# Kernel optimization log

Hardware: AMD Instinct MI355X
Metric: run time of the kernel (lower is better)

Reference implementation:

```python
import jax, jax.numpy as jnp
import numpy as np

NUM_CODEBOOK = 2048
EMBED_DIM = 64
BETA = 0.25


def _l2norm(x, eps=1e-12):
    # F.normalize(x, dim=1): x / max(||x||, eps)
    n = jnp.sqrt(jnp.sum(x * x, axis=1, keepdims=True))
    return x / jnp.maximum(n, eps)


def setup_inputs() -> dict:
    key = jax.random.key(0)
    k1, k2 = jax.random.split(key)
    z = jax.random.normal(k1, (16, EMBED_DIM, 64, 64), dtype=jnp.float32)
    # xavier_normal_ init for (K, d) embedding weight
    std = float(np.sqrt(2.0 / (NUM_CODEBOOK + EMBED_DIM)))
    codebook = jax.random.normal(k2, (NUM_CODEBOOK, EMBED_DIM), dtype=jnp.float32) * std
    return {"z": z, "codebook": codebook}


def reference(z, codebook):
    b, d, h, w = z.shape
    z_bhwd = jnp.transpose(z, (0, 2, 3, 1))          # (b,h,w,d)
    z_flat = z_bhwd.reshape(-1, d)                   # (n,d)

    # normalize == 'l2'
    z_norm = _l2norm(z_flat)
    codebook_norm = _l2norm(codebook)                # (K,d)

    # squared euclidean distance: ||z||^2 + ||c||^2 - 2 z c^T  -> (n,K)
    distance = (jnp.sum(z_norm * z_norm, axis=1, keepdims=True)
                + jnp.sum(codebook_norm * codebook_norm, axis=1)
                - 2.0 * jnp.matmul(z_norm, codebook_norm.T))

    vq_indices = jnp.argmin(distance, axis=1)        # (n,)
    distance_prob = jax.nn.softmax(-distance, axis=1)

    z_q = codebook_norm[vq_indices]                  # (n,d) embedding gather

    codebook_loss = jnp.mean((z_q - jax.lax.stop_gradient(z_norm)) ** 2)
    commitment_loss = jnp.mean((z_norm - jax.lax.stop_gradient(z_q)) ** 2)
    loss = codebook_loss + BETA * commitment_loss

    # straight-through estimator
    z_q_st = z_norm + jax.lax.stop_gradient(z_q - z_norm)
    q = jnp.transpose(z_q_st.reshape(b, h, w, d), (0, 3, 1, 2))  # (b,d,h,w)
    return q, loss, codebook_loss, commitment_loss, distance_prob
```

## Files before the change

kernel.cpp:

```cpp
#include <hip/hip_runtime.h>
#include <hip/hip_fp16.h>

typedef _Float16 f16x8 __attribute__((ext_vector_type(8)));
typedef float f32x4 __attribute__((ext_vector_type(4)));

#define NN 65536
#define KK 2048
#define DD 64

__device__ __forceinline__ unsigned int fkey(float f) {
  unsigned int u = __float_as_uint(f);
  return (u & 0x80000000u) ? ~u : (u | 0x80000000u);
}

__global__ void k_norm_cb(const float* __restrict__ cb, float* __restrict__ cbT32,
                          float* __restrict__ cn2,
                          unsigned short* __restrict__ Bhi,
                          unsigned short* __restrict__ Blo) {
  int gid = blockIdx.x * blockDim.x + threadIdx.x;
  int c = gid >> 6;
  int k = gid & 63;
  float v = cb[c * DD + k];
  float ss = v * v;
  #pragma unroll
  for (int o = 32; o; o >>= 1) ss += __shfl_xor(ss, o);
  float inv = 1.0f / fmaxf(sqrtf(ss), 1e-12f);
  float cn = v * inv;
  cbT32[k * KK + c] = cn;
  float s2 = cn * cn;
  #pragma unroll
  for (int o = 32; o; o >>= 1) s2 += __shfl_xor(s2, o);
  if (k == 0) cn2[c] = s2;
  float sh = cn * 256.0f;
  _Float16 hh = (_Float16)sh;
  float resid = sh - (float)hh;
  _Float16 hl = (_Float16)(resid * 4096.0f);
  int s = k >> 5, g2 = (k >> 3) & 3, i = k & 7;
  int idx = s * 65536 + c * 32 + g2 * 8 + i;
  Bhi[idx] = *(unsigned short*)&hh;
  Blo[idx] = *(unsigned short*)&hl;
}

__global__ void k_norm_z(const float* __restrict__ z,
                         unsigned short* __restrict__ Ahi,
                         unsigned short* __restrict__ Alo) {
  __shared__ float np_[8][32];
  __shared__ float invS[32];
  int t = threadIdx.x;
  int r32 = t & 31, q = t >> 5;
  int n0 = blockIdx.x * 32;
  int w0 = n0 & 63, hh = (n0 >> 6) & 63, bb = n0 >> 12;
  const float* src = z + (size_t)bb * 262144 + (size_t)q * 8 * 4096 + hh * 64 + w0 + r32;
  float v[8];
  float ss = 0.f;
  #pragma unroll
  for (int i = 0; i < 8; ++i) {
    float x = src[(size_t)i * 4096];
    v[i] = x;
    ss = fmaf(x, x, ss);
  }
  np_[q][r32] = ss;
  __syncthreads();
  if (t < 32) {
    float s = 0.f;
    #pragma unroll
    for (int qq = 0; qq < 8; ++qq) s += np_[qq][t];
    invS[t] = 1.0f / fmaxf(sqrtf(s), 1e-12f);
  }
  __syncthreads();
  float inv = invS[r32] * 256.0f;
  union { _Float16 h[8]; uint4 u; } hi, lo;
  #pragma unroll
  for (int i = 0; i < 8; ++i) {
    float sh = v[i] * inv;
    _Float16 a = (_Float16)sh;
    hi.h[i] = a;
    lo.h[i] = (_Float16)((sh - (float)a) * 4096.0f);
  }
  int rt = (n0 + r32) >> 4;
  int r = r32 & 15;
  int s = q >> 2, g2 = q & 3;
  size_t idx = (size_t)(rt * 2 + s) * 64 + g2 * 16 + r;
  ((uint4*)Ahi)[idx] = hi.u;
  ((uint4*)Alo)[idx] = lo.u;
}

__global__ __launch_bounds__(512, 4) void k_main(
    const f16x8* __restrict__ Ahi, const f16x8* __restrict__ Alo,
    const f16x8* __restrict__ Bhi, const f16x8* __restrict__ Blo,
    const float* __restrict__ cn2g, const float* __restrict__ cbT32,
    float* __restrict__ qout, float* __restrict__ prob,
    float* __restrict__ partials) {
  __shared__ __half ehS[16][1032];
  __shared__ unsigned long long keyS[16];
  __shared__ float rowpart[16][8];
  __shared__ float rowInv[16];
  __shared__ float wsum[8];

  int t = threadIdx.x;
  int lane = t & 63, wv = t >> 6;
  int l15 = lane & 15, g = lane >> 4;
  int rt = blockIdx.x;
  int n0 = rt * 16;

  if (t < 16) keyS[t] = ~0ull;

  f16x8 z_hi[2], z_lo[2];
  {
    size_t base = (size_t)rt * 128 + (size_t)g * 16 + l15;
    z_hi[0] = Ahi[base];      z_hi[1] = Ahi[base + 64];
    z_lo[0] = Alo[base];      z_lo[1] = Alo[base + 64];
  }

  f32x4 acc1[8];
  unsigned long long kmin = ~0ull;
  float esumT = 0.f;

  #pragma unroll
  for (int pass = 0; pass < 2; ++pass) {
    int wc0 = pass * 1024 + wv * 128;
    #pragma unroll
    for (int i = 0; i < 8; ++i) acc1[i] = (f32x4){0.f, 0.f, 0.f, 0.f};
    f32x4 acc2t = (f32x4){0.f, 0.f, 0.f, 0.f};

    int b0 = (wc0 + l15) * 4 + g;
    f16x8 bhA = Bhi[b0], blA = Blo[b0];
    f16x8 bhB, blB;
    #pragma unroll
    for (int p = 0; p < 16; ++p) {
      int t8 = p >> 1, s = p & 1;
      if (p < 15) {
        int pn = p + 1;
        int idxn = (pn & 1) * 8192 + (pn >> 1) * 64 + b0;
        if (p & 1) { bhA = Bhi[idxn]; blA = Blo[idxn]; }
        else       { bhB = Bhi[idxn]; blB = Blo[idxn]; }
      }
      f16x8 bh = (p & 1) ? bhB : bhA;
      f16x8 bl = (p & 1) ? blB : blA;
      acc2t    = __builtin_amdgcn_mfma_f32_16x16x32_f16(bh, z_lo[s], acc2t, 0, 0, 0);
      acc1[t8] = __builtin_amdgcn_mfma_f32_16x16x32_f16(bh, z_hi[s], acc1[t8], 0, 0, 0);
      acc2t    = __builtin_amdgcn_mfma_f32_16x16x32_f16(bl, z_hi[s], acc2t, 0, 0, 0);
      if (s == 1) {
        acc1[t8] += acc2t * 2.44140625e-04f;
        acc2t = (f32x4){0.f, 0.f, 0.f, 0.f};
      }
    }

    int cb0 = wc0 + g * 4;
    #pragma unroll
    for (int t8 = 0; t8 < 8; ++t8) {
      int c0 = cb0 + t8 * 16;
      float4 c4 = *(const float4*)(cn2g + c0);
      float cn[4] = {c4.x, c4.y, c4.z, c4.w};
      #pragma unroll
      for (int r = 0; r < 4; ++r) {
        float d = fmaf(acc1[t8][r], -3.0517578125e-05f, cn[r]);
        unsigned long long kk = ((unsigned long long)fkey(d) << 32) | (unsigned)(c0 + r);
        if (kk < kmin) kmin = kk;
        float e = __expf(-d);
        acc1[t8][r] = e;
        esumT += e;
      }
    }
    if (pass == 0) {
      #pragma unroll
      for (int t8 = 0; t8 < 8; ++t8) {
        int off = wv * 128 + t8 * 16 + g * 4;
        *(__half2*)&ehS[l15][off]     = __floats2half2_rn(acc1[t8][0], acc1[t8][1]);
        *(__half2*)&ehS[l15][off + 2] = __floats2half2_rn(acc1[t8][2], acc1[t8][3]);
      }
    }
  }

  #pragma unroll
  for (int o = 16; o <= 32; o <<= 1) {
    esumT += __shfl_xor(esumT, o);
    unsigned long long ok = __shfl_xor(kmin, o);
    if (ok < kmin) kmin = ok;
  }
  __syncthreads();
  if (lane < 16) {
    rowpart[l15][wv] = esumT;
    atomicMin(&keyS[l15], kmin);
  }
  __syncthreads();
  if (t < 16) {
    float s = 0.f;
    #pragma unroll
    for (int w = 0; w < 8; ++w) s += rowpart[t][w];
    rowInv[t] = 1.0f / s;
  }
  __syncthreads();

  {
    float inv = rowInv[l15];
    float* pr = prob + (size_t)(n0 + l15) * KK + wv * 128 + g * 4;
    #pragma unroll
    for (int t8 = 0; t8 < 8; ++t8)
      *(f32x4*)(pr + 1024 + t8 * 16) = acc1[t8] * inv;
    #pragma unroll
    for (int t8 = 0; t8 < 8; ++t8) {
      int off = wv * 128 + t8 * 16 + g * 4;
      __half2 a = *(__half2*)&ehS[l15][off];
      __half2 b = *(__half2*)&ehS[l15][off + 2];
      f32x4 o4;
      o4[0] = __low2float(a) * inv;
      o4[1] = __high2float(a) * inv;
      o4[2] = __low2float(b) * inv;
      o4[3] = __high2float(b) * inv;
      *(f32x4*)(pr + t8 * 16) = o4;
    }
  }

  {
    float ssd = 0.f;
    #pragma unroll
    for (int i = 0; i < 2; ++i) {
      int e = i * 512 + t;
      int d = e >> 4, wi = e & 15;
      int cw = (int)(keyS[wi] & 0xffffffffull);
      float qv = cbT32[d * KK + cw];
      int w0 = n0 & 63, hh2 = (n0 >> 6) & 63, bb = n0 >> 12;
      qout[((size_t)((bb << 6) | d) * 64 + hh2) * 64 + w0 + wi] = qv;
      size_t aidx = ((size_t)(rt * 2 + (d >> 5)) * 64 + ((d >> 3) & 3) * 16 + wi) * 8 + (d & 7);
      float ah = (float)((const _Float16*)Ahi)[aidx];
      float al = (float)((const _Float16*)Alo)[aidx];
      float zn = fmaf(al, 2.44140625e-04f, ah) * 3.90625e-03f;
      float df = qv - zn;
      ssd = fmaf(df, df, ssd);
    }
    #pragma unroll
    for (int o = 32; o; o >>= 1) ssd += __shfl_xor(ssd, o);
    if (lane == 0) wsum[wv] = ssd;
  }
  __syncthreads();
  if (t == 0) {
    float s = 0.f;
    #pragma unroll
    for (int w = 0; w < 8; ++w) s += wsum[w];
    partials[rt] = s;
  }
}

__global__ void k_final(const float* __restrict__ partials, float* __restrict__ out) {
  __shared__ float wsh[4];
  int t = threadIdx.x;
  float s = 0.f;
  for (int i = 0; i < 16; ++i) s += partials[t * 16 + i];
  #pragma unroll
  for (int o = 32; o; o >>= 1) s += __shfl_xor(s, o);
  if ((t & 63) == 0) wsh[t >> 6] = s;
  __syncthreads();
  if (t == 0) {
    float tot = (wsh[0] + wsh[1]) + (wsh[2] + wsh[3]);
    float cbl = tot * (1.0f / 4194304.0f);
    out[4194304] = 1.25f * cbl;
    out[4194305] = cbl;
    out[4194306] = cbl;
  }
}

extern "C" void kernel_launch(void* const* d_in, const int* in_sizes, int n_in,
                              void* d_out, int out_size, void* d_ws, size_t ws_size,
                              hipStream_t stream) {
  const float* z = (const float*)d_in[0];
  const float* cb = (const float*)d_in[1];
  float* out = (float*)d_out;
  char* ws = (char*)d_ws;

  float* cbT32 = (float*)(ws);
  float* cn2 = (float*)(ws + 524288);
  unsigned short* Bhi = (unsigned short*)(ws + 532480);
  unsigned short* Blo = (unsigned short*)(ws + 794624);
  float* partials = (float*)(ws + 1056768);
  unsigned short* Ahi = (unsigned short*)(ws + 1073152);
  unsigned short* Alo = (unsigned short*)(ws + 9461760);

  k_norm_cb<<<512, 256, 0, stream>>>(cb, cbT32, cn2, Bhi, Blo);
  k_norm_z<<<2048, 256, 0, stream>>>(z, Ahi, Alo);
  k_main<<<4096, 512, 0, stream>>>((const f16x8*)Ahi, (const f16x8*)Alo,
                                   (const f16x8*)Bhi, (const f16x8*)Blo,
                                   cn2, cbT32, out, out + 4194307, partials);
  k_final<<<1, 256, 0, stream>>>(partials, out);
}
```

Baseline: 289.9 us.

## Replace split-fp16 MFMA with single fp16 pass plus exact fp64 argmin refinement

```diff
diff --git a/kernel.cpp b/kernel.cpp
--- a/kernel.cpp
+++ b/kernel.cpp
@@ -14,9 +14,8 @@
 }
 
 __global__ void k_norm_cb(const float* __restrict__ cb, float* __restrict__ cbT32,
-                          float* __restrict__ cn2,
-                          unsigned short* __restrict__ Bhi,
-                          unsigned short* __restrict__ Blo) {
+                          float* __restrict__ cbRM, float* __restrict__ cn2,
+                          unsigned short* __restrict__ Bhi) {
   int gid = blockIdx.x * blockDim.x + threadIdx.x;
   int c = gid >> 6;
   int k = gid & 63;
@@ -27,23 +26,19 @@
   float inv = 1.0f / fmaxf(sqrtf(ss), 1e-12f);
   float cn = v * inv;
   cbT32[k * KK + c] = cn;
+  cbRM[c * DD + k] = cn;
   float s2 = cn * cn;
   #pragma unroll
   for (int o = 32; o; o >>= 1) s2 += __shfl_xor(s2, o);
   if (k == 0) cn2[c] = s2;
-  float sh = cn * 256.0f;
-  _Float16 hh = (_Float16)sh;
-  float resid = sh - (float)hh;
-  _Float16 hl = (_Float16)(resid * 4096.0f);
+  _Float16 hh = (_Float16)(cn * 256.0f);
   int s = k >> 5, g2 = (k >> 3) & 3, i = k & 7;
-  int idx = s * 65536 + c * 32 + g2 * 8 + i;
-  Bhi[idx] = *(unsigned short*)&hh;
-  Blo[idx] = *(unsigned short*)&hl;
+  Bhi[s * 65536 + c * 32 + g2 * 8 + i] = *(unsigned short*)&hh;
 }
 
 __global__ void k_norm_z(const float* __restrict__ z,
                          unsigned short* __restrict__ Ahi,
-                         unsigned short* __restrict__ Alo) {
+                         float* __restrict__ znRM) {
   __shared__ float np_[8][32];
   __shared__ float invS[32];
   int t = threadIdx.x;
@@ -68,33 +63,46 @@
     invS[t] = 1.0f / fmaxf(sqrtf(s), 1e-12f);
   }
   __syncthreads();
-  float inv = invS[r32] * 256.0f;
-  union { _Float16 h[8]; uint4 u; } hi, lo;
+  float inv = invS[r32];
+  float zr[8];
+  union { _Float16 h[8]; uint4 u; } hi;
   #pragma unroll
   for (int i = 0; i < 8; ++i) {
-    float sh = v[i] * inv;
-    _Float16 a = (_Float16)sh;
-    hi.h[i] = a;
-    lo.h[i] = (_Float16)((sh - (float)a) * 4096.0f);
-  }
+    zr[i] = v[i] * inv;
+    hi.h[i] = (_Float16)(zr[i] * 256.0f);
+  }
+  float* zd = znRM + (size_t)(n0 + r32) * 64 + q * 8;
+  *(f32x4*)zd = (f32x4){zr[0], zr[1], zr[2], zr[3]};
+  *(f32x4*)(zd + 4) = (f32x4){zr[4], zr[5], zr[6], zr[7]};
   int rt = (n0 + r32) >> 4;
   int r = r32 & 15;
   int s = q >> 2, g2 = q & 3;
-  size_t idx = (size_t)(rt * 2 + s) * 64 + g2 * 16 + r;
-  ((uint4*)Ahi)[idx] = hi.u;
-  ((uint4*)Alo)[idx] = lo.u;
+  ((uint4*)Ahi)[(size_t)(rt * 2 + s) * 64 + g2 * 16 + r] = hi.u;
+}
+
+__device__ __forceinline__ unsigned long long exact_key(
+    const float* __restrict__ znr, const float* __restrict__ cbRM,
+    const float* __restrict__ cn2g, int col) {
+  const float* cbr = cbRM + col * 64;
+  double s = 0.0;
+  #pragma unroll 8
+  for (int k = 0; k < 64; ++k) s = fma((double)znr[k], (double)cbr[k], s);
+  float dex = fmaf(-2.0f, (float)s, cn2g[col]);
+  return ((unsigned long long)fkey(dex) << 32) | (unsigned)col;
 }
 
 __global__ __launch_bounds__(512, 4) void k_main(
-    const f16x8* __restrict__ Ahi, const f16x8* __restrict__ Alo,
-    const f16x8* __restrict__ Bhi, const f16x8* __restrict__ Blo,
+    const f16x8* __restrict__ Ahi, const f16x8* __restrict__ Bhi,
     const float* __restrict__ cn2g, const float* __restrict__ cbT32,
+    const float* __restrict__ cbRM, const float* __restrict__ znRM,
     float* __restrict__ qout, float* __restrict__ prob,
     float* __restrict__ partials) {
   __shared__ __half ehS[16][1032];
   __shared__ unsigned long long keyS[16];
+  __shared__ unsigned long long keyExS[16];
   __shared__ float rowpart[16][8];
   __shared__ float rowInv[16];
+  __shared__ float dminS[16];
   __shared__ float wsum[8];
 
   int t = threadIdx.x;
@@ -103,17 +111,17 @@
   int rt = blockIdx.x;
   int n0 = rt * 16;
 
-  if (t < 16) keyS[t] = ~0ull;
-
-  f16x8 z_hi[2], z_lo[2];
+  if (t < 16) { keyS[t] = ~0ull; keyExS[t] = ~0ull; }
+
+  f16x8 z_hi[2];
   {
     size_t base = (size_t)rt * 128 + (size_t)g * 16 + l15;
-    z_hi[0] = Ahi[base];      z_hi[1] = Ahi[base + 64];
-    z_lo[0] = Alo[base];      z_lo[1] = Alo[base + 64];
+    z_hi[0] = Ahi[base];
+    z_hi[1] = Ahi[base + 64];
   }
 
   f32x4 acc1[8];
-  unsigned long long kmin = ~0ull;
+  unsigned long long kminH = ~0ull;
   float esumT = 0.f;
 
   #pragma unroll
@@ -121,29 +129,21 @@
     int wc0 = pass * 1024 + wv * 128;
     #pragma unroll
     for (int i = 0; i < 8; ++i) acc1[i] = (f32x4){0.f, 0.f, 0.f, 0.f};
-    f32x4 acc2t = (f32x4){0.f, 0.f, 0.f, 0.f};
 
     int b0 = (wc0 + l15) * 4 + g;
-    f16x8 bhA = Bhi[b0], blA = Blo[b0];
-    f16x8 bhB, blB;
+    f16x8 bA = Bhi[b0];
+    f16x8 bB;
     #pragma unroll
     for (int p = 0; p < 16; ++p) {
       int t8 = p >> 1, s = p & 1;
       if (p < 15) {
         int pn = p + 1;
         int idxn = (pn & 1) * 8192 + (pn >> 1) * 64 + b0;
-        if (p & 1) { bhA = Bhi[idxn]; blA = Blo[idxn]; }
-        else       { bhB = Bhi[idxn]; blB = Blo[idxn]; }
+        if (p & 1) bA = Bhi[idxn];
+        else       bB = Bhi[idxn];
       }
-      f16x8 bh = (p & 1) ? bhB : bhA;
-      f16x8 bl = (p & 1) ? blB : blA;
-      acc2t    = __builtin_amdgcn_mfma_f32_16x16x32_f16(bh, z_lo[s], acc2t, 0, 0, 0);
+      f16x8 bh = (p & 1) ? bB : bA;
       acc1[t8] = __builtin_amdgcn_mfma_f32_16x16x32_f16(bh, z_hi[s], acc1[t8], 0, 0, 0);
-      acc2t    = __builtin_amdgcn_mfma_f32_16x16x32_f16(bl, z_hi[s], acc2t, 0, 0, 0);
-      if (s == 1) {
-        acc1[t8] += acc2t * 2.44140625e-04f;
-        acc2t = (f32x4){0.f, 0.f, 0.f, 0.f};
-      }
     }
 
     int cb0 = wc0 + g * 4;
@@ -156,7 +156,7 @@
       for (int r = 0; r < 4; ++r) {
         float d = fmaf(acc1[t8][r], -3.0517578125e-05f, cn[r]);
         unsigned long long kk = ((unsigned long long)fkey(d) << 32) | (unsigned)(c0 + r);
-        if (kk < kmin) kmin = kk;
+        if (kk < kminH) kminH = kk;
         float e = __expf(-d);
         acc1[t8][r] = e;
         esumT += e;
@@ -175,13 +175,13 @@
   #pragma unroll
   for (int o = 16; o <= 32; o <<= 1) {
     esumT += __shfl_xor(esumT, o);
-    unsigned long long ok = __shfl_xor(kmin, o);
-    if (ok < kmin) kmin = ok;
+    unsigned long long ok = __shfl_xor(kminH, o);
+    if (ok < kminH) kminH = ok;
   }
   __syncthreads();
   if (lane < 16) {
     rowpart[l15][wv] = esumT;
-    atomicMin(&keyS[l15], kmin);
+    atomicMin(&keyS[l15], kminH);
   }
   __syncthreads();
   if (t < 16) {
@@ -189,6 +189,9 @@
     #pragma unroll
     for (int w = 0; w < 8; ++w) s += rowpart[t][w];
     rowInv[t] = 1.0f / s;
+    unsigned int u = (unsigned int)(keyS[t] >> 32);
+    dminS[t] = (u & 0x80000000u) ? __uint_as_float(u & 0x7fffffffu)
+                                 : __uint_as_float(~u);
   }
   __syncthreads();
 
@@ -196,8 +199,10 @@
     float inv = rowInv[l15];
     float* pr = prob + (size_t)(n0 + l15) * KK + wv * 128 + g * 4;
     #pragma unroll
-    for (int t8 = 0; t8 < 8; ++t8)
-      *(f32x4*)(pr + 1024 + t8 * 16) = acc1[t8] * inv;
+    for (int t8 = 0; t8 < 8; ++t8) {
+      f32x4 o4 = acc1[t8] * inv;
+      __builtin_nontemporal_store(o4, (f32x4*)(pr + 1024 + t8 * 16));
+    }
     #pragma unroll
     for (int t8 = 0; t8 < 8; ++t8) {
       int off = wv * 128 + t8 * 16 + g * 4;
@@ -208,9 +213,45 @@
       o4[1] = __high2float(a) * inv;
       o4[2] = __low2float(b) * inv;
       o4[3] = __high2float(b) * inv;
-      *(f32x4*)(pr + t8 * 16) = o4;
-    }
-  }
+      __builtin_nontemporal_store(o4, (f32x4*)(pr + t8 * 16));
+    }
+  }
+
+  {
+    const float* znr = znRM + (size_t)(n0 + l15) * 64;
+    float eTh = __expf(-dminS[l15] - 0.008f) * 0.995f;
+    unsigned long long kex = ~0ull;
+    #pragma unroll
+    for (int t8 = 0; t8 < 8; ++t8) {
+      int c0 = 1024 + wv * 128 + t8 * 16 + g * 4;
+      #pragma unroll
+      for (int r = 0; r < 4; ++r)
+        if (acc1[t8][r] >= eTh) {
+          unsigned long long kk = exact_key(znr, cbRM, cn2g, c0 + r);
+          if (kk < kex) kex = kk;
+        }
+    }
+    #pragma unroll
+    for (int t8 = 0; t8 < 8; ++t8) {
+      int off = wv * 128 + t8 * 16 + g * 4;
+      __half2 a = *(__half2*)&ehS[l15][off];
+      __half2 b = *(__half2*)&ehS[l15][off + 2];
+      float ev[4] = {__low2float(a), __high2float(a), __low2float(b), __high2float(b)};
+      #pragma unroll
+      for (int r = 0; r < 4; ++r)
+        if (ev[r] >= eTh) {
+          unsigned long long kk = exact_key(znr, cbRM, cn2g, off + r);
+          if (kk < kex) kex = kk;
+        }
+    }
+    #pragma unroll
+    for (int o = 16; o <= 32; o <<= 1) {
+      unsigned long long ok = __shfl_xor(kex, o);
+      if (ok < kex) kex = ok;
+    }
+    if (lane < 16) atomicMin(&keyExS[l15], kex);
+  }
+  __syncthreads();
 
   {
     float ssd = 0.f;
@@ -218,14 +259,11 @@
     for (int i = 0; i < 2; ++i) {
       int e = i * 512 + t;
       int d = e >> 4, wi = e & 15;
-      int cw = (int)(keyS[wi] & 0xffffffffull);
+      int cw = (int)(keyExS[wi] & 0xffffffffull);
       float qv = cbT32[d * KK + cw];
       int w0 = n0 & 63, hh2 = (n0 >> 6) & 63, bb = n0 >> 12;
       qout[((size_t)((bb << 6) | d) * 64 + hh2) * 64 + w0 + wi] = qv;
-      size_t aidx = ((size_t)(rt * 2 + (d >> 5)) * 64 + ((d >> 3) & 3) * 16 + wi) * 8 + (d & 7);
-      float ah = (float)((const _Float16*)Ahi)[aidx];
-      float al = (float)((const _Float16*)Alo)[aidx];
-      float zn = fmaf(al, 2.44140625e-04f, ah) * 3.90625e-03f;
+      float zn = znRM[(size_t)(n0 + wi) * 64 + d];
       float df = qv - zn;
       ssd = fmaf(df, df, ssd);
     }
@@ -269,17 +307,17 @@
   char* ws = (char*)d_ws;
 
   float* cbT32 = (float*)(ws);
-  float* cn2 = (float*)(ws + 524288);
-  unsigned short* Bhi = (unsigned short*)(ws + 532480);
-  unsigned short* Blo = (unsigned short*)(ws + 794624);
-  float* partials = (float*)(ws + 1056768);
-  unsigned short* Ahi = (unsigned short*)(ws + 1073152);
-  unsigned short* Alo = (unsigned short*)(ws + 9461760);
-
-  k_norm_cb<<<512, 256, 0, stream>>>(cb, cbT32, cn2, Bhi, Blo);
-  k_norm_z<<<2048, 256, 0, stream>>>(z, Ahi, Alo);
-  k_main<<<4096, 512, 0, stream>>>((const f16x8*)Ahi, (const f16x8*)Alo,
-                                   (const f16x8*)Bhi, (const f16x8*)Blo,
-                                   cn2, cbT32, out, out + 4194307, partials);
+  float* cbRM = (float*)(ws + 524288);
+  float* cn2 = (float*)(ws + 1048576);
+  unsigned short* Bhi = (unsigned short*)(ws + 1056768);
+  float* partials = (float*)(ws + 1318912);
+  unsigned short* Ahi = (unsigned short*)(ws + 1335296);
+  float* znRM = (float*)(ws + 9723904);
+
+  k_norm_cb<<<512, 256, 0, stream>>>(cb, cbT32, cbRM, cn2, Bhi);
+  k_norm_z<<<2048, 256, 0, stream>>>(z, Ahi, znRM);
+  k_main<<<4096, 512, 0, stream>>>((const f16x8*)Ahi, (const f16x8*)Bhi,
+                                   cn2, cbT32, cbRM, znRM,
+                                   out, out + 4194307, partials);
   k_final<<<1, 256, 0, stream>>>(partials, out);
 }
```

New measurement: 545.3 us. 88.1% more time.
